# Optimization experiments

Hardware: AMD Instinct MI355X
Metric: run time of the kernel (lower is better)

## Reference

```python
import jax, jax.numpy as jnp
import numpy as np

B, S, D = 64, 512, 768


def setup_inputs() -> dict:
    key = jax.random.key(0)
    k1, k2, k3 = jax.random.split(key, 3)
    topic_embedding = jax.random.normal(k1, (B, D), dtype=jnp.float32)
    sequence_embedding = jax.random.normal(k2, (B, S, D), dtype=jnp.float32)
    # Shared bilinear scoring layer parameters: score = t^T W x + b (scalar per pair)
    W = jax.random.normal(k3, (D, D), dtype=jnp.float32) / np.sqrt(D)
    b = jnp.zeros((1,), dtype=jnp.float32)
    return {"topic_embedding": topic_embedding, "sequence_embedding": sequence_embedding, "W": W, "b": b}


def reference(topic_embedding, sequence_embedding, W, b):
    # Original: per-batch map_fn applying bilinear layer to (topic repeated over S, seq tokens),
    # then softmax over the sequence dimension. Fully batched here:
    # scores[b, s] = topic[b] @ W @ seq[b, s] + bias
    tW = topic_embedding @ W                       # [B, D]
    scores = jnp.einsum('bd,bsd->bs', tW, sequence_embedding) + b[0]  # [B, S]
    beta = jax.nn.softmax(scores, axis=-1)         # [B, S]
    return beta
```

## Files before the change

kernel.cpp:

```cpp
#include <hip/hip_runtime.h>

#define BB 64
#define SS 512
#define DD 768
#define D4 192
#define BG 4

typedef float v4f __attribute__((ext_vector_type(4)));

__global__ void tw_kernel(const float* __restrict__ topic,
                          const float* __restrict__ W,
                          float* __restrict__ tW) {
    __shared__ float t_s[BG][DD];
    __shared__ float4 red[16][BG][16];
    const int t  = threadIdx.x;
    const int b0 = blockIdx.x * BG;
    const int d4 = blockIdx.y * 16;
    const int dl = t & 15;
    const int kg = t >> 4;

#pragma unroll
    for (int bi = 0; bi < BG; ++bi)
        for (int k = t; k < DD; k += 256) t_s[bi][k] = topic[(b0 + bi) * DD + k];
    __syncthreads();

    const float4* __restrict__ W4 = (const float4*)W;
    const int k0 = kg * 48;
    float4 acc[BG];
#pragma unroll
    for (int bi = 0; bi < BG; ++bi) acc[bi] = make_float4(0.f, 0.f, 0.f, 0.f);

#pragma unroll 8
    for (int k = 0; k < 48; ++k) {
        const float4 w = W4[(size_t)(k0 + k) * D4 + d4 + dl];
#pragma unroll
        for (int bi = 0; bi < BG; ++bi) {
            const float ts = t_s[bi][k0 + k];
            acc[bi].x = fmaf(ts, w.x, acc[bi].x);
            acc[bi].y = fmaf(ts, w.y, acc[bi].y);
            acc[bi].z = fmaf(ts, w.z, acc[bi].z);
            acc[bi].w = fmaf(ts, w.w, acc[bi].w);
        }
    }
#pragma unroll
    for (int bi = 0; bi < BG; ++bi) red[kg][bi][dl] = acc[bi];
    __syncthreads();

    if (t < 64) {
        const int bi = t >> 4, d = t & 15;
        float4 s = red[0][bi][d];
#pragma unroll
        for (int j = 1; j < 16; ++j) {
            const float4 r = red[j][bi][d];
            s.x += r.x; s.y += r.y; s.z += r.z; s.w += r.w;
        }
        ((float4*)tW)[(size_t)(b0 + bi) * D4 + d4 + d] = s;
    }
}

__global__ void score_kernel(const float* __restrict__ tW,
                             const float* __restrict__ seq,
                             const float* __restrict__ bias,
                             float* __restrict__ scores) {
    const int gwid = (int)((blockIdx.x * blockDim.x + threadIdx.x) >> 6);
    const int lane = threadIdx.x & 63;
    const int b = gwid >> 8;
    const int s = (gwid & 255) << 1;

    const v4f* sp = (const v4f*)(seq + ((size_t)b * SS + s) * DD);
    const float4* tp = (const float4*)(tW + (size_t)b * DD);

    float a0 = 0.f, a1 = 0.f;
#pragma unroll
    for (int k = 0; k < 3; ++k) {
        const float4 t = tp[lane + k * 64];
        const v4f x0 = __builtin_nontemporal_load(sp + lane + k * 64);
        const v4f x1 = __builtin_nontemporal_load(sp + D4 + lane + k * 64);
        a0 = fmaf(x0.x, t.x, a0);
        a0 = fmaf(x0.y, t.y, a0);
        a0 = fmaf(x0.z, t.z, a0);
        a0 = fmaf(x0.w, t.w, a0);
        a1 = fmaf(x1.x, t.x, a1);
        a1 = fmaf(x1.y, t.y, a1);
        a1 = fmaf(x1.z, t.z, a1);
        a1 = fmaf(x1.w, t.w, a1);
    }
#pragma unroll
    for (int off = 32; off >= 1; off >>= 1) {
        a0 += __shfl_xor(a0, off);
        a1 += __shfl_xor(a1, off);
    }

    if (lane == 0) {
        const float bb = bias[0];
        scores[b * SS + s]     = a0 + bb;
        scores[b * SS + s + 1] = a1 + bb;
    }
}

__global__ void softmax_kernel(const float* __restrict__ scores,
                               float* __restrict__ beta) {
    __shared__ float red[8];
    __shared__ float s_m, s_sum;
    const int b   = blockIdx.x;
    const int tid = threadIdx.x;
    const int wid = tid >> 6, lane = tid & 63;

    const float v = scores[b * SS + tid];

    float m = v;
#pragma unroll
    for (int off = 32; off >= 1; off >>= 1) m = fmaxf(m, __shfl_xor(m, off));
    if (lane == 0) red[wid] = m;
    __syncthreads();
    if (tid == 0) {
        float mm = red[0];
#pragma unroll
        for (int i = 1; i < 8; ++i) mm = fmaxf(mm, red[i]);
        s_m = mm;
    }
    __syncthreads();

    const float e = __expf(v - s_m);
    float sum = e;
#pragma unroll
    for (int off = 32; off >= 1; off >>= 1) sum += __shfl_xor(sum, off);
    if (lane == 0) red[wid] = sum;
    __syncthreads();
    if (tid == 0) {
        float ss = 0.f;
#pragma unroll
        for (int i = 0; i < 8; ++i) ss += red[i];
        s_sum = ss;
    }
    __syncthreads();

    beta[b * SS + tid] = e / s_sum;
}

extern "C" void kernel_launch(void* const* d_in, const int* in_sizes, int n_in,
                              void* d_out, int out_size, void* d_ws, size_t ws_size,
                              hipStream_t stream) {
    const float* topic = (const float*)d_in[0];
    const float* seq   = (const float*)d_in[1];
    const float* W     = (const float*)d_in[2];
    const float* bias  = (const float*)d_in[3];
    float* out = (float*)d_out;

    float* tW     = (float*)d_ws;
    float* scores = tW + (size_t)BB * DD;

    tw_kernel<<<dim3(BB / BG, 12), 256, 0, stream>>>(topic, W, tW);

    const int total_waves = (BB * SS) / 2;
    const int blocks = (total_waves * 64) / 256;
    score_kernel<<<blocks, 256, 0, stream>>>(tW, seq, bias, scores);

    softmax_kernel<<<BB, 512, 0, stream>>>(scores, out);
}
```

Measured before the change: 33.57 us.

## Split tW reduction over K chunks and fold partial sums into score kernel

The topic@W kernel now splits the K dimension into four chunks across a third grid dimension, giving four times more blocks, and writes partial tW vectors instead of a final sum. The score kernel sums those four partials on the fly while computing dot products, and now assigns one sequence row per wave instead of two. The aim is to fill more of the GPU during the small tW stage and to cut per-wave work in the score stage. In exchange, each score wave reads four times as much tW data (mostly from cache), and twice as many waves are launched.

```diff
diff --git a/kernel.cpp b/kernel.cpp
--- a/kernel.cpp
+++ b/kernel.cpp
@@ -5,37 +5,38 @@
 #define DD 768
 #define D4 192
 #define BG 4
+#define KC 4
 
 typedef float v4f __attribute__((ext_vector_type(4)));
 
-__global__ void tw_kernel(const float* __restrict__ topic,
-                          const float* __restrict__ W,
-                          float* __restrict__ tW) {
-    __shared__ float t_s[BG][DD];
+__global__ void tw_part_kernel(const float* __restrict__ topic,
+                               const float* __restrict__ W,
+                               float* __restrict__ part) {
+    __shared__ float t_s[BG][192];
     __shared__ float4 red[16][BG][16];
     const int t  = threadIdx.x;
     const int b0 = blockIdx.x * BG;
     const int d4 = blockIdx.y * 16;
+    const int k0 = blockIdx.z * 192;
     const int dl = t & 15;
     const int kg = t >> 4;
 
-#pragma unroll
-    for (int bi = 0; bi < BG; ++bi)
-        for (int k = t; k < DD; k += 256) t_s[bi][k] = topic[(b0 + bi) * DD + k];
+    for (int i = t; i < BG * 192; i += 256)
+        t_s[i / 192][i % 192] = topic[(b0 + i / 192) * DD + k0 + (i % 192)];
     __syncthreads();
 
     const float4* __restrict__ W4 = (const float4*)W;
-    const int k0 = kg * 48;
+    const int kk0 = kg * 12;
     float4 acc[BG];
 #pragma unroll
     for (int bi = 0; bi < BG; ++bi) acc[bi] = make_float4(0.f, 0.f, 0.f, 0.f);
 
-#pragma unroll 8
-    for (int k = 0; k < 48; ++k) {
-        const float4 w = W4[(size_t)(k0 + k) * D4 + d4 + dl];
+#pragma unroll
+    for (int k = 0; k < 12; ++k) {
+        const float4 w = W4[(size_t)(k0 + kk0 + k) * D4 + d4 + dl];
 #pragma unroll
         for (int bi = 0; bi < BG; ++bi) {
-            const float ts = t_s[bi][k0 + k];
+            const float ts = t_s[bi][kk0 + k];
             acc[bi].x = fmaf(ts, w.x, acc[bi].x);
             acc[bi].y = fmaf(ts, w.y, acc[bi].y);
             acc[bi].z = fmaf(ts, w.z, acc[bi].z);
@@ -54,48 +55,43 @@
             const float4 r = red[j][bi][d];
             s.x += r.x; s.y += r.y; s.z += r.z; s.w += r.w;
         }
-        ((float4*)tW)[(size_t)(b0 + bi) * D4 + d4 + d] = s;
+        ((float4*)part)[((size_t)blockIdx.z * BB + b0 + bi) * D4 + d4 + d] = s;
     }
 }
 
-__global__ void score_kernel(const float* __restrict__ tW,
+__global__ void score_kernel(const float* __restrict__ part,
                              const float* __restrict__ seq,
                              const float* __restrict__ bias,
                              float* __restrict__ scores) {
     const int gwid = (int)((blockIdx.x * blockDim.x + threadIdx.x) >> 6);
     const int lane = threadIdx.x & 63;
-    const int b = gwid >> 8;
-    const int s = (gwid & 255) << 1;
+    const int b = gwid >> 9;
+    const int s = gwid & (SS - 1);
 
     const v4f* sp = (const v4f*)(seq + ((size_t)b * SS + s) * DD);
-    const float4* tp = (const float4*)(tW + (size_t)b * DD);
+    const float4* pp = (const float4*)part;
 
-    float a0 = 0.f, a1 = 0.f;
+    v4f x[3];
 #pragma unroll
-    for (int k = 0; k < 3; ++k) {
-        const float4 t = tp[lane + k * 64];
-        const v4f x0 = __builtin_nontemporal_load(sp + lane + k * 64);
-        const v4f x1 = __builtin_nontemporal_load(sp + D4 + lane + k * 64);
-        a0 = fmaf(x0.x, t.x, a0);
-        a0 = fmaf(x0.y, t.y, a0);
-        a0 = fmaf(x0.z, t.z, a0);
-        a0 = fmaf(x0.w, t.w, a0);
-        a1 = fmaf(x1.x, t.x, a1);
-        a1 = fmaf(x1.y, t.y, a1);
-        a1 = fmaf(x1.z, t.z, a1);
-        a1 = fmaf(x1.w, t.w, a1);
+    for (int k = 0; k < 3; ++k) x[k] = __builtin_nontemporal_load(sp + lane + k * 64);
+
+    float acc = 0.f;
+#pragma unroll
+    for (int kc = 0; kc < KC; ++kc) {
+        const float4* tp = pp + ((size_t)kc * BB + b) * D4;
+#pragma unroll
+        for (int k = 0; k < 3; ++k) {
+            const float4 tv = tp[lane + k * 64];
+            acc = fmaf(x[k].x, tv.x, acc);
+            acc = fmaf(x[k].y, tv.y, acc);
+            acc = fmaf(x[k].z, tv.z, acc);
+            acc = fmaf(x[k].w, tv.w, acc);
+        }
     }
 #pragma unroll
-    for (int off = 32; off >= 1; off >>= 1) {
-        a0 += __shfl_xor(a0, off);
-        a1 += __shfl_xor(a1, off);
-    }
+    for (int off = 32; off >= 1; off >>= 1) acc += __shfl_xor(acc, off);
 
-    if (lane == 0) {
-        const float bb = bias[0];
-        scores[b * SS + s]     = a0 + bb;
-        scores[b * SS + s + 1] = a1 + bb;
-    }
+    if (lane == 0) scores[gwid] = acc + bias[0];
 }
 
 __global__ void softmax_kernel(const float* __restrict__ scores,
@@ -147,14 +143,14 @@
     const float* bias  = (const float*)d_in[3];
     float* out = (float*)d_out;
 
-    float* tW     = (float*)d_ws;
-    float* scores = tW + (size_t)BB * DD;
+    float* part   = (float*)d_ws;
+    float* scores = part + (size_t)KC * BB * DD;
 
-    tw_kernel<<<dim3(BB / BG, 12), 256, 0, stream>>>(topic, W, tW);
+    tw_part_kernel<<<dim3(BB / BG, 12, KC), 256, 0, stream>>>(topic, W, part);
 
-    const int total_waves = (BB * SS) / 2;
+    const int total_waves = BB * SS;
     const int blocks = (total_waves * 64) / 256;
-    score_kernel<<<blocks, 256, 0, stream>>>(tW, seq, bias, scores);
+    score_kernel<<<blocks, 256, 0, stream>>>(part, seq, bias, scores);
 
     softmax_kernel<<<BB, 512, 0, stream>>>(scores, out);
 }
```

New measurement: 35.89 us. +6.9%, slower.

## Widen tW grid with shuffle reductions and stage tW in LDS for scoring

Applied to the files above, without the earlier changes.

The tW kernel now gives each block 4 float4 columns instead of 16, which raises the grid from 192 to 768 blocks. Each thread covers 12 k-steps, partial sums are reduced with wave shuffles before a small LDS combine, and the topic load is vectorised. The score kernel now loads tW once per block into LDS. Each wave then processes 4 sequence rows with one full-row dot product and reduction per row, instead of 2 rows with tW read from global memory. The aim is better occupancy and less redundant tW traffic, in exchange for more shuffle work and more serialised per-row reductions.

```diff
diff --git a/kernel.cpp b/kernel.cpp
--- a/kernel.cpp
+++ b/kernel.cpp
@@ -12,26 +12,32 @@
                           const float* __restrict__ W,
                           float* __restrict__ tW) {
     __shared__ float t_s[BG][DD];
-    __shared__ float4 red[16][BG][16];
-    const int t  = threadIdx.x;
-    const int b0 = blockIdx.x * BG;
-    const int d4 = blockIdx.y * 16;
-    const int dl = t & 15;
-    const int kg = t >> 4;
+    __shared__ float4 red[4][BG][4];
+    const int t    = threadIdx.x;
+    const int b0   = blockIdx.x * BG;
+    const int d4   = blockIdx.y * 4;
+    const int dl   = t & 3;
+    const int kg   = t >> 2;
+    const int wv   = t >> 6;
+    const int lane = t & 63;
 
-#pragma unroll
-    for (int bi = 0; bi < BG; ++bi)
-        for (int k = t; k < DD; k += 256) t_s[bi][k] = topic[(b0 + bi) * DD + k];
+    {
+        const float4* tp  = (const float4*)topic + (size_t)b0 * D4;
+        float4*       ts4 = (float4*)t_s;
+        ts4[t]       = tp[t];
+        ts4[t + 256] = tp[t + 256];
+        ts4[t + 512] = tp[t + 512];
+    }
     __syncthreads();
 
     const float4* __restrict__ W4 = (const float4*)W;
-    const int k0 = kg * 48;
+    const int k0 = kg * 12;
     float4 acc[BG];
 #pragma unroll
     for (int bi = 0; bi < BG; ++bi) acc[bi] = make_float4(0.f, 0.f, 0.f, 0.f);
 
-#pragma unroll 8
-    for (int k = 0; k < 48; ++k) {
+#pragma unroll
+    for (int k = 0; k < 12; ++k) {
         const float4 w = W4[(size_t)(k0 + k) * D4 + d4 + dl];
 #pragma unroll
         for (int bi = 0; bi < BG; ++bi) {
@@ -42,18 +48,32 @@
             acc[bi].w = fmaf(ts, w.w, acc[bi].w);
         }
     }
+
 #pragma unroll
-    for (int bi = 0; bi < BG; ++bi) red[kg][bi][dl] = acc[bi];
+    for (int off = 4; off <= 32; off <<= 1) {
+#pragma unroll
+        for (int bi = 0; bi < BG; ++bi) {
+            acc[bi].x += __shfl_xor(acc[bi].x, off);
+            acc[bi].y += __shfl_xor(acc[bi].y, off);
+            acc[bi].z += __shfl_xor(acc[bi].z, off);
+            acc[bi].w += __shfl_xor(acc[bi].w, off);
+        }
+    }
+    if (lane < 4) {
+#pragma unroll
+        for (int bi = 0; bi < BG; ++bi) red[wv][bi][lane] = acc[bi];
+    }
     __syncthreads();
 
-    if (t < 64) {
-        const int bi = t >> 4, d = t & 15;
-        float4 s = red[0][bi][d];
-#pragma unroll
-        for (int j = 1; j < 16; ++j) {
-            const float4 r = red[j][bi][d];
-            s.x += r.x; s.y += r.y; s.z += r.z; s.w += r.w;
-        }
+    if (t < 16) {
+        const int bi = t >> 2, d = t & 3;
+        const float4 s0 = red[0][bi][d], s1 = red[1][bi][d];
+        const float4 s2 = red[2][bi][d], s3 = red[3][bi][d];
+        float4 s;
+        s.x = (s0.x + s1.x) + (s2.x + s3.x);
+        s.y = (s0.y + s1.y) + (s2.y + s3.y);
+        s.z = (s0.z + s1.z) + (s2.z + s3.z);
+        s.w = (s0.w + s1.w) + (s2.w + s3.w);
         ((float4*)tW)[(size_t)(b0 + bi) * D4 + d4 + d] = s;
     }
 }
@@ -62,39 +82,40 @@
                              const float* __restrict__ seq,
                              const float* __restrict__ bias,
                              float* __restrict__ scores) {
-    const int gwid = (int)((blockIdx.x * blockDim.x + threadIdx.x) >> 6);
-    const int lane = threadIdx.x & 63;
-    const int b = gwid >> 8;
-    const int s = (gwid & 255) << 1;
+    __shared__ float4 t_lds[D4];
+    const int t     = threadIdx.x;
+    const int b     = blockIdx.x >> 5;
+    const int chunk = blockIdx.x & 31;
+    const int wv    = t >> 6, lane = t & 63;
 
-    const v4f* sp = (const v4f*)(seq + ((size_t)b * SS + s) * DD);
-    const float4* tp = (const float4*)(tW + (size_t)b * DD);
+    if (t < D4) t_lds[t] = ((const float4*)tW)[(size_t)b * D4 + t];
+    __syncthreads();
 
-    float a0 = 0.f, a1 = 0.f;
+    const float4 t0 = t_lds[lane];
+    const float4 t1 = t_lds[lane + 64];
+    const float4 t2 = t_lds[lane + 128];
+
+    const int s0 = chunk * 16 + wv * 4;
 #pragma unroll
-    for (int k = 0; k < 3; ++k) {
-        const float4 t = tp[lane + k * 64];
-        const v4f x0 = __builtin_nontemporal_load(sp + lane + k * 64);
-        const v4f x1 = __builtin_nontemporal_load(sp + D4 + lane + k * 64);
-        a0 = fmaf(x0.x, t.x, a0);
-        a0 = fmaf(x0.y, t.y, a0);
-        a0 = fmaf(x0.z, t.z, a0);
-        a0 = fmaf(x0.w, t.w, a0);
-        a1 = fmaf(x1.x, t.x, a1);
-        a1 = fmaf(x1.y, t.y, a1);
-        a1 = fmaf(x1.z, t.z, a1);
-        a1 = fmaf(x1.w, t.w, a1);
-    }
+    for (int i = 0; i < 4; ++i) {
+        const int s = s0 + i;
+        const v4f* sp = (const v4f*)(seq + ((size_t)b * SS + s) * DD);
+        const v4f x0 = __builtin_nontemporal_load(sp + lane);
+        const v4f x1 = __builtin_nontemporal_load(sp + lane + 64);
+        const v4f x2 = __builtin_nontemporal_load(sp + lane + 128);
+
+        float acc = 0.f;
+        acc = fmaf(x0.x, t0.x, acc); acc = fmaf(x0.y, t0.y, acc);
+        acc = fmaf(x0.z, t0.z, acc); acc = fmaf(x0.w, t0.w, acc);
+        acc = fmaf(x1.x, t1.x, acc); acc = fmaf(x1.y, t1.y, acc);
+        acc = fmaf(x1.z, t1.z, acc); acc = fmaf(x1.w, t1.w, acc);
+        acc = fmaf(x2.x, t2.x, acc); acc = fmaf(x2.y, t2.y, acc);
+        acc = fmaf(x2.z, t2.z, acc); acc = fmaf(x2.w, t2.w, acc);
+
 #pragma unroll
-    for (int off = 32; off >= 1; off >>= 1) {
-        a0 += __shfl_xor(a0, off);
-        a1 += __shfl_xor(a1, off);
-    }
+        for (int off = 32; off >= 1; off >>= 1) acc += __shfl_xor(acc, off);
 
-    if (lane == 0) {
-        const float bb = bias[0];
-        scores[b * SS + s]     = a0 + bb;
-        scores[b * SS + s + 1] = a1 + bb;
+        if (lane == 0) scores[(size_t)b * SS + s] = acc + bias[0];
     }
 }
 
@@ -150,11 +171,9 @@
     float* tW     = (float*)d_ws;
     float* scores = tW + (size_t)BB * DD;
 
-    tw_kernel<<<dim3(BB / BG, 12), 256, 0, stream>>>(topic, W, tW);
+    tw_kernel<<<dim3(BB / BG, DD / 16), 256, 0, stream>>>(topic, W, tW);
 
-    const int total_waves = (BB * SS) / 2;
-    const int blocks = (total_waves * 64) / 256;
-    score_kernel<<<blocks, 256, 0, stream>>>(tW, seq, bias, scores);
+    score_kernel<<<BB * (SS / 16), 256, 0, stream>>>(tW, seq, bias, scores);
 
     softmax_kernel<<<BB, 512, 0, stream>>>(scores, out);
 }
```

Measured after the change: 31.40 us. 1.07x faster.
